# Kernel optimization log

Measured on AMD Instinct MI355X. Metric: run time of the kernel, lower is better.

The kernel has to match this reference:

```python
import jax, jax.numpy as jnp
import numpy as np

LN_EPS = 1e-5

def _layernorm(x, g, b):
    mu = jnp.mean(x, axis=-1, keepdims=True)
    var = jnp.var(x, axis=-1, keepdims=True)
    return (x - mu) * jax.lax.rsqrt(var + LN_EPS) * g + b

def setup_inputs() -> dict:
    key = jax.random.key(0)
    ks = jax.random.split(key, 5)
    N, M, A, B = 30000, 12, 256, 128
    atom_feats = jax.random.normal(ks[0], (N, A), dtype=jnp.float32)
    bond_feats = jax.random.normal(ks[1], (N, M, B), dtype=jnp.float32)
    fc_w = jax.random.normal(ks[2], (2 * A, 2 * A + B), dtype=jnp.float32) * 0.02
    fc_b = jax.random.normal(ks[3], (2 * A,), dtype=jnp.float32) * 0.02
    ln1_g = jnp.ones((2 * A,), dtype=jnp.float32)
    ln1_b = jnp.zeros((2 * A,), dtype=jnp.float32)
    ln2_g = jnp.ones((A,), dtype=jnp.float32)
    ln2_b = jnp.zeros((A,), dtype=jnp.float32)
    nbr_indices = jax.random.randint(ks[4], (N, M), 0, N, dtype=jnp.int64)
    return {"atom_feats": atom_feats, "bond_feats": bond_feats, "fc_w": fc_w,
            "fc_b": fc_b, "ln1_g": ln1_g, "ln1_b": ln1_b, "ln2_g": ln2_g,
            "ln2_b": ln2_b, "nbr_indices": nbr_indices}

def reference(atom_feats, bond_feats, fc_w, fc_b, ln1_g, ln1_b, ln2_g, ln2_b, nbr_indices):
    N, M = nbr_indices.shape
    A = atom_feats.shape[-1]
    nbr_feats = atom_feats[nbr_indices]                        # [N, M, A] gather
    atom_expand = jnp.broadcast_to(atom_feats[:, None, :], (N, M, A))
    combined = jnp.concatenate([atom_expand, nbr_feats, bond_feats], axis=-1)  # [N, M, 2A+B]
    z = jnp.einsum('nmd,kd->nmk', combined, fc_w) + fc_b       # [N, M, 2A]
    z = _layernorm(z, ln1_g, ln1_b)
    gate = jax.nn.sigmoid(z[..., :A])
    core = jax.nn.softplus(z[..., A:])
    out = jnp.mean(gate * core, axis=1)                        # [N, A]
    out = _layernorm(out, ln2_g, ln2_b)
    return atom_feats + out
```

## Files before the change

kernel.cpp:

```cpp
#include <hip/hip_runtime.h>
#include <hip/hip_bf16.h>

#define N_ATOMS 30000
#define M_NBR   12

typedef __bf16 bf16x8 __attribute__((ext_vector_type(8)));
typedef float  f32x4  __attribute__((ext_vector_type(4)));

__device__ __forceinline__ unsigned pkbf(float a, float b) {
    union { __bf16 h[2]; unsigned u; } r;
    r.h[0] = (__bf16)a; r.h[1] = (__bf16)b;
    return r.u;
}
__device__ __forceinline__ unsigned short f2bf(float f) {
    union { __bf16 h; unsigned short s; } r; r.h = (__bf16)f; return r.s;
}
__device__ __forceinline__ float bflo(unsigned u) { union { unsigned x; float f; } v; v.x = u << 16;          return v.f; }
__device__ __forceinline__ float bfhi(unsigned u) { union { unsigned x; float f; } v; v.x = u & 0xffff0000u;  return v.f; }

__device__ __forceinline__ float fexp2(float x) { return __builtin_amdgcn_exp2f(x); }
__device__ __forceinline__ float flog2(float x) { return __builtin_amdgcn_logf(x); }

__device__ __forceinline__ float rowsum16(float x) {
    union { float f; int i; } a, b;
    a.f = x;
    b.i = __builtin_amdgcn_update_dpp(0, a.i, 0x121, 0xF, 0xF, true); a.f += b.f;
    b.i = __builtin_amdgcn_update_dpp(0, a.i, 0x122, 0xF, 0xF, true); a.f += b.f;
    b.i = __builtin_amdgcn_update_dpp(0, a.i, 0x124, 0xF, 0xF, true); a.f += b.f;
    b.i = __builtin_amdgcn_update_dpp(0, a.i, 0x128, 0xF, 0xF, true); a.f += b.f;
    return a.f;
}

__device__ __forceinline__ int packAddr8(int c) {
    int cc = c & 255;
    int slot = ((cc >> 4) & 1) + ((c >> 8) << 1);
    return (cc >> 5) * 64 + (cc & 15) * 4 + slot;
}

__global__ void pack_weights(const float* __restrict__ fc_w,
                             unsigned short* __restrict__ Wp1,
                             unsigned short* __restrict__ Wp3) {
    int idx = blockIdx.x * 256 + threadIdx.x;
    const int n1 = 32 * 1024 * 8;
    if (idx < n1) {
        int j = idx & 7, n = (idx >> 3) & 1023, g = idx >> 13;
        float v = (n < 512) ? fc_w[n * 640 + g * 8 + j]
                            : fc_w[(n - 512) * 640 + 256 + g * 8 + j];
        Wp1[idx] = f2bf(v);
    } else {
        int k = idx - n1;
        if (k < 16 * 512 * 8) {
            int j = k & 7, n = (k >> 3) & 511, g = k >> 12;
            Wp3[k] = f2bf(fc_w[n * 640 + 512 + g * 8 + j]);
        }
    }
}

__global__ __launch_bounds__(512, 2) void gemm_p(
    const float* __restrict__ atom, const float* __restrict__ fc_b,
    const unsigned short* __restrict__ Wp1, unsigned short* __restrict__ P)
{
    __shared__ unsigned short sA[128 * 256];
    const int tid = threadIdx.x;
    const int r0 = blockIdx.x * 128;
    const int cb = blockIdx.y;

    #pragma unroll
    for (int s = 0; s < 8; ++s) {
        int G = tid + s * 512;
        int row = G >> 5, gc = G & 31;
        int grow = r0 + row;
        uint4 pk;
        if (grow < N_ATOMS) {
            const float4* src = reinterpret_cast<const float4*>(atom + (size_t)grow * 256 + gc * 8);
            float4 v0 = src[0], v1 = src[1];
            pk.x = pkbf(v0.x, v0.y); pk.y = pkbf(v0.z, v0.w);
            pk.z = pkbf(v1.x, v1.y); pk.w = pkbf(v1.z, v1.w);
        } else {
            pk = make_uint4(0u, 0u, 0u, 0u);
        }
        *reinterpret_cast<uint4*>(&sA[row * 256 + ((gc ^ (row & 7)) << 3)]) = pk;
    }
    __syncthreads();

    const int lane = tid & 63, wave = tid >> 6;
    const int wr = wave >> 2, wcc = wave & 3;
    const int l15 = lane & 15, l16 = lane >> 4;

    f32x4 acc[4][8];
    #pragma unroll
    for (int mt = 0; mt < 4; ++mt)
        #pragma unroll
        for (int nt = 0; nt < 8; ++nt) acc[mt][nt] = f32x4{0.f, 0.f, 0.f, 0.f};

    #pragma unroll
    for (int ks = 0; ks < 8; ++ks) {
        bf16x8 af[4];
        #pragma unroll
        for (int mt = 0; mt < 4; ++mt) {
            int row = wr * 64 + mt * 16 + l15;
            int g = ks * 4 + l16;
            af[mt] = *reinterpret_cast<const bf16x8*>(&sA[row * 256 + ((g ^ (row & 7)) << 3)]);
        }
        bf16x8 bfr[8];
        #pragma unroll
        for (int nt = 0; nt < 8; ++nt) {
            int col = cb * 512 + wcc * 128 + nt * 16 + l15;
            bfr[nt] = *reinterpret_cast<const bf16x8*>(&Wp1[((size_t)(ks * 4 + l16) * 1024 + col) * 8]);
        }
        #pragma unroll
        for (int mt = 0; mt < 4; ++mt)
            #pragma unroll
            for (int nt = 0; nt < 8; ++nt)
                acc[mt][nt] = __builtin_amdgcn_mfma_f32_16x16x32_bf16(af[mt], bfr[nt], acc[mt][nt], 0, 0, 0);
    }

    #pragma unroll
    for (int np = 0; np < 4; ++np) {
        int zc0 = wcc * 128 + np * 32 + l15;
        float b0 = (cb == 0) ? fc_b[zc0] : 0.f;
        float b1 = (cb == 0) ? fc_b[zc0 + 16] : 0.f;
        int pa = cb * 512 + packAddr8(zc0);
        #pragma unroll
        for (int mt = 0; mt < 4; ++mt) {
            #pragma unroll
            for (int j = 0; j < 4; ++j) {
                int row = r0 + wr * 64 + mt * 16 + l16 * 4 + j;
                if (row < N_ATOMS)
                    *reinterpret_cast<unsigned*>(&P[(size_t)row * 1024 + pa]) =
                        pkbf(acc[mt][2 * np][j] + b0, acc[mt][2 * np + 1][j] + b1);
            }
        }
    }
}

__global__ __launch_bounds__(256, 4) void fused_conv(
    const float* __restrict__ atom, const float* __restrict__ bond,
    const int* __restrict__ nbr, const unsigned short* __restrict__ P,
    const unsigned short* __restrict__ Wp3,
    const float* __restrict__ ln1_g, const float* __restrict__ ln1_b,
    const float* __restrict__ ln2_g, const float* __restrict__ ln2_b,
    float* __restrict__ out)
{
    __shared__ unsigned short sA[32 * 128];
    __shared__ __align__(16) float sRed[2][32][4];
    __shared__ __align__(16) float sL2[2][2][4];

    const int tid = threadIdx.x;
    const int i0 = blockIdx.x * 2;
    const int lane = tid & 63, wc = tid >> 6;
    const int l15 = lane & 15, l16 = lane >> 4;
    const float L2E = 1.4426950408889634f;
    const char* Pb = reinterpret_cast<const char*>(P);
    const unsigned cOffA = (unsigned)(wc * 256 + l15 * 8);
    const unsigned cOffB = cOffA + 128u;

    float4 bv[3];
    #pragma unroll
    for (int s = 0; s < 3; ++s) {
        int g = tid + s * 256;
        int row = g >> 5, gc = g & 31;
        bv[s] = *reinterpret_cast<const float4*>(bond + (size_t)(i0 * 12 + row) * 128 + gc * 4);
    }

    int4 nbq0 = *reinterpret_cast<const int4*>(&nbr[i0 * 12 + l16 * 4]);
    int off16 = (l16 < 2) ? (16 + l16 * 4) : 20;
    int4 nbq1 = *reinterpret_cast<const int4*>(&nbr[i0 * 12 + off16]);

    uint2 p2q[2][4][2];
    {
        const int* n0 = reinterpret_cast<const int*>(&nbq0);
        const int* n1 = reinterpret_cast<const int*>(&nbq1);
        #pragma unroll
        for (int j = 0; j < 4; ++j) {
            unsigned b0 = (unsigned)n0[j] * 2048u + 1024u;
            p2q[0][j][0] = *reinterpret_cast<const uint2*>(Pb + b0 + cOffA);
            p2q[0][j][1] = *reinterpret_cast<const uint2*>(Pb + b0 + cOffB);
            unsigned b1 = (unsigned)n1[j] * 2048u + 1024u;
            p2q[1][j][0] = *reinterpret_cast<const uint2*>(Pb + b1 + cOffA);
            p2q[1][j][1] = *reinterpret_cast<const uint2*>(Pb + b1 + cOffB);
        }
    }
    uint2 p1q[2][2];
    {
        unsigned a0 = (unsigned)(i0 + ((l16 < 3) ? 0 : 1)) * 2048u;
        p1q[0][0] = *reinterpret_cast<const uint2*>(Pb + a0 + cOffA);
        p1q[0][1] = *reinterpret_cast<const uint2*>(Pb + a0 + cOffB);
        unsigned a1 = (unsigned)(i0 + 1) * 2048u;
        p1q[1][0] = *reinterpret_cast<const uint2*>(Pb + a1 + cOffA);
        p1q[1][1] = *reinterpret_cast<const uint2*>(Pb + a1 + cOffB);
    }

    #pragma unroll
    for (int s = 0; s < 3; ++s) {
        int g = tid + s * 256;
        int row = g >> 5, gc = g & 31;
        uint2 pk;
        pk.x = pkbf(bv[s].x, bv[s].y); pk.y = pkbf(bv[s].z, bv[s].w);
        int elem = (((gc >> 1) ^ (row & 7)) << 3) + ((gc & 1) << 2);
        *reinterpret_cast<uint2*>(&sA[row * 128 + elem]) = pk;
    }
    {
        int row = 24 + (tid >> 5), gc = tid & 31;
        *reinterpret_cast<uint2*>(&sA[row * 128 + gc * 4]) = make_uint2(0u, 0u);
    }

    f32x4 acc[2][8];
    #pragma unroll
    for (int mt = 0; mt < 2; ++mt)
        #pragma unroll
        for (int np = 0; np < 2; ++np) {
            uint2 c1 = p1q[mt][np];
            float pg0 = bflo(c1.x), pg1 = bfhi(c1.x);
            float pc0 = bflo(c1.y), pc1 = bfhi(c1.y);
            #pragma unroll
            for (int j = 0; j < 4; ++j) {
                uint2 c2 = p2q[mt][j][np];
                acc[mt][np * 2 + 0][j]     = pg0 + bflo(c2.x);
                acc[mt][np * 2 + 1][j]     = pg1 + bfhi(c2.x);
                acc[mt][4 + np * 2 + 0][j] = pc0 + bflo(c2.y);
                acc[mt][4 + np * 2 + 1][j] = pc1 + bfhi(c2.y);
            }
        }
    __syncthreads();

    #pragma unroll
    for (int ks = 0; ks < 4; ++ks) {
        bf16x8 af[2];
        #pragma unroll
        for (int mt = 0; mt < 2; ++mt) {
            int row = mt * 16 + l15;
            af[mt] = *reinterpret_cast<const bf16x8*>(
                &sA[row * 128 + (((ks * 4 + l16) ^ (row & 7)) << 3)]);
        }
        #pragma unroll
        for (int p = 0; p < 2; ++p)
            #pragma unroll
            for (int np = 0; np < 2; ++np) {
                int colbase = p * 256 + wc * 64 + np * 32 + l15;
                bf16x8 b0 = *reinterpret_cast<const bf16x8*>(
                    &Wp3[((size_t)(ks * 4 + l16) * 512 + colbase) * 8]);
                bf16x8 b1 = *reinterpret_cast<const bf16x8*>(
                    &Wp3[((size_t)(ks * 4 + l16) * 512 + colbase + 16) * 8]);
                #pragma unroll
                for (int mt = 0; mt < 2; ++mt) {
                    acc[mt][p * 4 + np * 2 + 0] = __builtin_amdgcn_mfma_f32_16x16x32_bf16(
                        af[mt], b0, acc[mt][p * 4 + np * 2 + 0], 0, 0, 0);
                    acc[mt][p * 4 + np * 2 + 1] = __builtin_amdgcn_mfma_f32_16x16x32_bf16(
                        af[mt], b1, acc[mt][p * 4 + np * 2 + 1], 0, 0, 0);
                }
            }
    }

    #pragma unroll
    for (int mt = 0; mt < 2; ++mt)
        #pragma unroll
        for (int j = 0; j < 4; ++j) {
            int row = mt * 16 + l16 * 4 + j;
            float s = 0.f, q = 0.f;
            #pragma unroll
            for (int nt = 0; nt < 8; ++nt) {
                float z = acc[mt][nt][j];
                s += z; q = fmaf(z, z, q);
            }
            s = rowsum16(s);
            q = rowsum16(q);
            if (l15 == 0) { sRed[0][row][wc] = s; sRed[1][row][wc] = q; }
        }

    float g1[4], gC[4], l2b1[4], l2bC[4];
    #pragma unroll
    for (int np = 0; np < 2; ++np)
        #pragma unroll
        for (int b = 0; b < 2; ++b) {
            int nt = np * 2 + b;
            int a = wc * 64 + np * 32 + b * 16 + l15;
            g1[nt] = ln1_g[a];       l2b1[nt] = ln1_b[a] * L2E;
            gC[nt] = ln1_g[256 + a]; l2bC[nt] = ln1_b[256 + a] * L2E;
        }
    __syncthreads();

    float pa0[4] = {0.f, 0.f, 0.f, 0.f};
    float pa1[4] = {0.f, 0.f, 0.f, 0.f};
    #pragma unroll
    for (int mt = 0; mt < 2; ++mt) {
        float rs[4], mr[4];
        #pragma unroll
        for (int j = 0; j < 4; ++j) {
            int row = mt * 16 + l16 * 4 + j;
            float4 s4 = *reinterpret_cast<const float4*>(&sRed[0][row][0]);
            float4 q4 = *reinterpret_cast<const float4*>(&sRed[1][row][0]);
            float ssum = (s4.x + s4.y) + (s4.z + s4.w);
            float qsum = (q4.x + q4.y) + (q4.z + q4.w);
            float mu = ssum * (1.f / 512.f);
            float var = qsum * (1.f / 512.f) - mu * mu;
            float r = __builtin_amdgcn_rsqf(var + 1e-5f) * L2E;
            rs[j] = r; mr[j] = mu * r;
        }
        #pragma unroll
        for (int nt = 0; nt < 4; ++nt) {
            float tq = 0.f;
            #pragma unroll
            for (int j = 0; j < 4; ++j) {
                float ug = fmaf(fmaf(acc[mt][nt][j],     rs[j], -mr[j]), g1[nt], l2b1[nt]);
                float uc = fmaf(fmaf(acc[mt][nt + 4][j], rs[j], -mr[j]), gC[nt], l2bC[nt]);
                float gt  = __builtin_amdgcn_rcpf(1.f + fexp2(-ug));
                float sp2 = flog2(1.f + fexp2(uc));
                tq = fmaf(gt, sp2, tq);
            }
            if (mt == 0) {
                if (l16 < 3) pa0[nt] += tq; else pa1[nt] += tq;
            } else {
                if (l16 < 2) pa1[nt] += tq;
            }
        }
    }
    #pragma unroll
    for (int nt = 0; nt < 4; ++nt) {
        pa0[nt] += __shfl_xor(pa0[nt], 16, 64);
        pa0[nt] += __shfl_xor(pa0[nt], 32, 64);
        pa1[nt] += __shfl_xor(pa1[nt], 16, 64);
        pa1[nt] += __shfl_xor(pa1[nt], 32, 64);
    }

    {
        float s0 = (pa0[0] + pa0[1]) + (pa0[2] + pa0[3]);
        float q0 = fmaf(pa0[0], pa0[0], fmaf(pa0[1], pa0[1], fmaf(pa0[2], pa0[2], pa0[3] * pa0[3])));
        float s1 = (pa1[0] + pa1[1]) + (pa1[2] + pa1[3]);
        float q1 = fmaf(pa1[0], pa1[0], fmaf(pa1[1], pa1[1], fmaf(pa1[2], pa1[2], pa1[3] * pa1[3])));
        s0 = rowsum16(s0); q0 = rowsum16(q0);
        s1 = rowsum16(s1); q1 = rowsum16(q1);
        if (lane == 0) {
            sL2[0][0][wc] = s0; sL2[0][1][wc] = q0;
            sL2[1][0][wc] = s1; sL2[1][1][wc] = q1;
        }
    }
    __syncthreads();

    if (l16 < 2) {
        const int a = l16;
        const int gi = i0 + a;
        float4 sv = *reinterpret_cast<const float4*>(&sL2[a][0][0]);
        float4 qv = *reinterpret_cast<const float4*>(&sL2[a][1][0]);
        float ssum = (sv.x + sv.y) + (sv.z + sv.w);
        float qsum = (qv.x + qv.y) + (qv.z + qv.w);
        float mu = ssum * (1.f / 256.f);
        float var = qsum * (1.f / 256.f) - mu * mu;
        float rstd = __builtin_amdgcn_rsqf(var + 1e-5f);
        float vv[4];
        #pragma unroll
        for (int nt = 0; nt < 4; ++nt) vv[nt] = (l16 == 0) ? pa0[nt] : pa1[nt];
        #pragma unroll
        for (int np = 0; np < 2; ++np)
            #pragma unroll
            for (int b = 0; b < 2; ++b) {
                int nt = np * 2 + b;
                int c = wc * 64 + np * 32 + b * 16 + l15;
                out[(size_t)gi * 256 + c] = atom[(size_t)gi * 256 + c]
                                          + (vv[nt] - mu) * rstd * ln2_g[c] + ln2_b[c];
            }
    }
}

extern "C" void kernel_launch(void* const* d_in, const int* in_sizes, int n_in,
                              void* d_out, int out_size, void* d_ws, size_t ws_size,
                              hipStream_t stream) {
    const float* atom  = (const float*)d_in[0];
    const float* bond  = (const float*)d_in[1];
    const float* fc_w  = (const float*)d_in[2];
    const float* fc_b  = (const float*)d_in[3];
    const float* ln1_g = (const float*)d_in[4];
    const float* ln1_b = (const float*)d_in[5];
    const float* ln2_g = (const float*)d_in[6];
    const float* ln2_b = (const float*)d_in[7];
    const int*   nbr   = (const int*)d_in[8];

    char* ws = (char*)d_ws;
    unsigned short* P   = (unsigned short*)ws;
    unsigned short* Wp1 = (unsigned short*)(ws + 61440000);
    unsigned short* Wp3 = (unsigned short*)(ws + 61440000 + 524288);
    float* outp = (float*)d_out;

    hipLaunchKernelGGL(pack_weights, dim3(1280), dim3(256), 0, stream, fc_w, Wp1, Wp3);
    hipLaunchKernelGGL(gemm_p, dim3(235, 2), dim3(512), 0, stream, atom, fc_b, Wp1, P);
    hipLaunchKernelGGL(fused_conv, dim3(15000), dim3(256), 0, stream,
                       atom, bond, nbr, P, Wp3, ln1_g, ln1_b, ln2_g, ln2_b, outp);
}
```

Baseline: 239.7 us.

## Process one atom per block in fused_conv to cut registers and raise occupancy

The fused convolution kernel now handles a single atom (12 neighbor rows padded to 16) per block instead of two atoms (24 rows padded to 32). The grid doubles to 30000 blocks and the launch-bounds occupancy hint rises from 4 to 6. Accumulator and prefetch register arrays are halved and the reductions are simplified. The aim is more concurrent waves to hide gather latency. The cost is that each 16-row MFMA tile now does only 12 useful rows, against 24 of 32 before, and the weight fragments from Wp3 are reloaded twice as often per atom.

New measurement: 281.9 us. 1.18x slower.

```diff
diff --git a/kernel.cpp b/kernel.cpp
--- a/kernel.cpp
+++ b/kernel.cpp
@@ -134,7 +134,7 @@
     }
 }
 
-__global__ __launch_bounds__(256, 4) void fused_conv(
+__global__ __launch_bounds__(256, 6) void fused_conv(
     const float* __restrict__ atom, const float* __restrict__ bond,
     const int* __restrict__ nbr, const unsigned short* __restrict__ P,
     const unsigned short* __restrict__ Wp3,
@@ -142,12 +142,12 @@
     const float* __restrict__ ln2_g, const float* __restrict__ ln2_b,
     float* __restrict__ out)
 {
-    __shared__ unsigned short sA[32 * 128];
-    __shared__ __align__(16) float sRed[2][32][4];
-    __shared__ __align__(16) float sL2[2][2][4];
+    __shared__ unsigned short sA[16 * 128];
+    __shared__ __align__(16) float sRed[2][16][4];
+    __shared__ __align__(16) float sL2[2][4];
 
     const int tid = threadIdx.x;
-    const int i0 = blockIdx.x * 2;
+    const int gi = blockIdx.x;
     const int lane = tid & 63, wc = tid >> 6;
     const int l15 = lane & 15, l16 = lane >> 4;
     const float L2E = 1.4426950408889634f;
@@ -155,84 +155,71 @@
     const unsigned cOffA = (unsigned)(wc * 256 + l15 * 8);
     const unsigned cOffB = cOffA + 128u;
 
-    float4 bv[3];
-    #pragma unroll
-    for (int s = 0; s < 3; ++s) {
-        int g = tid + s * 256;
-        int row = g >> 5, gc = g & 31;
-        bv[s] = *reinterpret_cast<const float4*>(bond + (size_t)(i0 * 12 + row) * 128 + gc * 4);
-    }
-
-    int4 nbq0 = *reinterpret_cast<const int4*>(&nbr[i0 * 12 + l16 * 4]);
-    int off16 = (l16 < 2) ? (16 + l16 * 4) : 20;
-    int4 nbq1 = *reinterpret_cast<const int4*>(&nbr[i0 * 12 + off16]);
-
-    uint2 p2q[2][4][2];
-    {
-        const int* n0 = reinterpret_cast<const int*>(&nbq0);
-        const int* n1 = reinterpret_cast<const int*>(&nbq1);
+    float4 bv0, bv1;
+    {
+        int row = tid >> 5, gc = tid & 31;
+        bv0 = *reinterpret_cast<const float4*>(bond + (size_t)(gi * 12 + row) * 128 + gc * 4);
+    }
+    if (tid < 128) {
+        int g2 = tid + 256;
+        int r2 = g2 >> 5, c2 = g2 & 31;
+        bv1 = *reinterpret_cast<const float4*>(bond + (size_t)(gi * 12 + r2) * 128 + c2 * 4);
+    }
+
+    int off = (l16 < 3) ? (l16 * 4) : 8;
+    int4 nbq = *reinterpret_cast<const int4*>(&nbr[gi * 12 + off]);
+    uint2 p2q[4][2];
+    {
+        const int* nn = reinterpret_cast<const int*>(&nbq);
         #pragma unroll
         for (int j = 0; j < 4; ++j) {
-            unsigned b0 = (unsigned)n0[j] * 2048u + 1024u;
-            p2q[0][j][0] = *reinterpret_cast<const uint2*>(Pb + b0 + cOffA);
-            p2q[0][j][1] = *reinterpret_cast<const uint2*>(Pb + b0 + cOffB);
-            unsigned b1 = (unsigned)n1[j] * 2048u + 1024u;
-            p2q[1][j][0] = *reinterpret_cast<const uint2*>(Pb + b1 + cOffA);
-            p2q[1][j][1] = *reinterpret_cast<const uint2*>(Pb + b1 + cOffB);
-        }
-    }
-    uint2 p1q[2][2];
-    {
-        unsigned a0 = (unsigned)(i0 + ((l16 < 3) ? 0 : 1)) * 2048u;
-        p1q[0][0] = *reinterpret_cast<const uint2*>(Pb + a0 + cOffA);
-        p1q[0][1] = *reinterpret_cast<const uint2*>(Pb + a0 + cOffB);
-        unsigned a1 = (unsigned)(i0 + 1) * 2048u;
-        p1q[1][0] = *reinterpret_cast<const uint2*>(Pb + a1 + cOffA);
-        p1q[1][1] = *reinterpret_cast<const uint2*>(Pb + a1 + cOffB);
-    }
-
-    #pragma unroll
-    for (int s = 0; s < 3; ++s) {
-        int g = tid + s * 256;
-        int row = g >> 5, gc = g & 31;
+            unsigned b = (unsigned)nn[j] * 2048u + 1024u;
+            p2q[j][0] = *reinterpret_cast<const uint2*>(Pb + b + cOffA);
+            p2q[j][1] = *reinterpret_cast<const uint2*>(Pb + b + cOffB);
+        }
+    }
+    uint2 p1qA = *reinterpret_cast<const uint2*>(Pb + (unsigned)gi * 2048u + cOffA);
+    uint2 p1qB = *reinterpret_cast<const uint2*>(Pb + (unsigned)gi * 2048u + cOffB);
+
+    {
+        int row = tid >> 5, gc = tid & 31;
         uint2 pk;
-        pk.x = pkbf(bv[s].x, bv[s].y); pk.y = pkbf(bv[s].z, bv[s].w);
+        pk.x = pkbf(bv0.x, bv0.y); pk.y = pkbf(bv0.z, bv0.w);
         int elem = (((gc >> 1) ^ (row & 7)) << 3) + ((gc & 1) << 2);
         *reinterpret_cast<uint2*>(&sA[row * 128 + elem]) = pk;
     }
-    {
-        int row = 24 + (tid >> 5), gc = tid & 31;
-        *reinterpret_cast<uint2*>(&sA[row * 128 + gc * 4]) = make_uint2(0u, 0u);
-    }
-
-    f32x4 acc[2][8];
-    #pragma unroll
-    for (int mt = 0; mt < 2; ++mt)
-        #pragma unroll
-        for (int np = 0; np < 2; ++np) {
-            uint2 c1 = p1q[mt][np];
-            float pg0 = bflo(c1.x), pg1 = bfhi(c1.x);
-            float pc0 = bflo(c1.y), pc1 = bfhi(c1.y);
-            #pragma unroll
-            for (int j = 0; j < 4; ++j) {
-                uint2 c2 = p2q[mt][j][np];
-                acc[mt][np * 2 + 0][j]     = pg0 + bflo(c2.x);
-                acc[mt][np * 2 + 1][j]     = pg1 + bfhi(c2.x);
-                acc[mt][4 + np * 2 + 0][j] = pc0 + bflo(c2.y);
-                acc[mt][4 + np * 2 + 1][j] = pc1 + bfhi(c2.y);
-            }
-        }
+    if (tid < 128) {
+        int g2 = tid + 256;
+        int r2 = g2 >> 5, c2 = g2 & 31;
+        uint2 pk2;
+        pk2.x = pkbf(bv1.x, bv1.y); pk2.y = pkbf(bv1.z, bv1.w);
+        int e2 = (((c2 >> 1) ^ (r2 & 7)) << 3) + ((c2 & 1) << 2);
+        *reinterpret_cast<uint2*>(&sA[r2 * 128 + e2]) = pk2;
+    }
+    *reinterpret_cast<unsigned*>(&sA[1536 + tid * 2]) = 0u;
+
+    f32x4 acc[8];
+    {
+        float pg0 = bflo(p1qA.x), pg1 = bfhi(p1qA.x);
+        float pc0 = bflo(p1qA.y), pc1 = bfhi(p1qA.y);
+        float qg0 = bflo(p1qB.x), qg1 = bfhi(p1qB.x);
+        float qc0 = bflo(p1qB.y), qc1 = bfhi(p1qB.y);
+        #pragma unroll
+        for (int j = 0; j < 4; ++j) {
+            uint2 cA = p2q[j][0], cB = p2q[j][1];
+            acc[0][j] = pg0 + bflo(cA.x); acc[1][j] = pg1 + bfhi(cA.x);
+            acc[4][j] = pc0 + bflo(cA.y); acc[5][j] = pc1 + bfhi(cA.y);
+            acc[2][j] = qg0 + bflo(cB.x); acc[3][j] = qg1 + bfhi(cB.x);
+            acc[6][j] = qc0 + bflo(cB.y); acc[7][j] = qc1 + bfhi(cB.y);
+        }
+    }
     __syncthreads();
 
     #pragma unroll
     for (int ks = 0; ks < 4; ++ks) {
-        bf16x8 af[2];
-        #pragma unroll
-        for (int mt = 0; mt < 2; ++mt) {
-            int row = mt * 16 + l15;
-            af[mt] = *reinterpret_cast<const bf16x8*>(
-                &sA[row * 128 + (((ks * 4 + l16) ^ (row & 7)) << 3)]);
-        }
+        int row = l15;
+        bf16x8 af = *reinterpret_cast<const bf16x8*>(
+            &sA[row * 128 + (((ks * 4 + l16) ^ (row & 7)) << 3)]);
         #pragma unroll
         for (int p = 0; p < 2; ++p)
             #pragma unroll
@@ -242,31 +229,26 @@
                     &Wp3[((size_t)(ks * 4 + l16) * 512 + colbase) * 8]);
                 bf16x8 b1 = *reinterpret_cast<const bf16x8*>(
                     &Wp3[((size_t)(ks * 4 + l16) * 512 + colbase + 16) * 8]);
-                #pragma unroll
-                for (int mt = 0; mt < 2; ++mt) {
-                    acc[mt][p * 4 + np * 2 + 0] = __builtin_amdgcn_mfma_f32_16x16x32_bf16(
-                        af[mt], b0, acc[mt][p * 4 + np * 2 + 0], 0, 0, 0);
-                    acc[mt][p * 4 + np * 2 + 1] = __builtin_amdgcn_mfma_f32_16x16x32_bf16(
-                        af[mt], b1, acc[mt][p * 4 + np * 2 + 1], 0, 0, 0);
-                }
+                acc[p * 4 + np * 2 + 0] = __builtin_amdgcn_mfma_f32_16x16x32_bf16(
+                    af, b0, acc[p * 4 + np * 2 + 0], 0, 0, 0);
+                acc[p * 4 + np * 2 + 1] = __builtin_amdgcn_mfma_f32_16x16x32_bf16(
+                    af, b1, acc[p * 4 + np * 2 + 1], 0, 0, 0);
             }
     }
 
     #pragma unroll
-    for (int mt = 0; mt < 2; ++mt)
-        #pragma unroll
-        for (int j = 0; j < 4; ++j) {
-            int row = mt * 16 + l16 * 4 + j;
-            float s = 0.f, q = 0.f;
-            #pragma unroll
-            for (int nt = 0; nt < 8; ++nt) {
-                float z = acc[mt][nt][j];
-                s += z; q = fmaf(z, z, q);
-            }
-            s = rowsum16(s);
-            q = rowsum16(q);
-            if (l15 == 0) { sRed[0][row][wc] = s; sRed[1][row][wc] = q; }
-        }
+    for (int j = 0; j < 4; ++j) {
+        int row = l16 * 4 + j;
+        float s = 0.f, q = 0.f;
+        #pragma unroll
+        for (int nt = 0; nt < 8; ++nt) {
+            float z = acc[nt][j];
+            s += z; q = fmaf(z, z, q);
+        }
+        s = rowsum16(s);
+        q = rowsum16(q);
+        if (l15 == 0) { sRed[0][row][wc] = s; sRed[1][row][wc] = q; }
+    }
 
     float g1[4], gC[4], l2b1[4], l2bC[4];
     #pragma unroll
@@ -280,85 +262,63 @@
         }
     __syncthreads();
 
-    float pa0[4] = {0.f, 0.f, 0.f, 0.f};
-    float pa1[4] = {0.f, 0.f, 0.f, 0.f};
-    #pragma unroll
-    for (int mt = 0; mt < 2; ++mt) {
-        float rs[4], mr[4];
+    float rs[4], mr[4];
+    #pragma unroll
+    for (int j = 0; j < 4; ++j) {
+        int row = l16 * 4 + j;
+        float4 s4 = *reinterpret_cast<const float4*>(&sRed[0][row][0]);
+        float4 q4 = *reinterpret_cast<const float4*>(&sRed[1][row][0]);
+        float ssum = (s4.x + s4.y) + (s4.z + s4.w);
+        float qsum = (q4.x + q4.y) + (q4.z + q4.w);
+        float mu = ssum * (1.f / 512.f);
+        float var = qsum * (1.f / 512.f) - mu * mu;
+        float r = __builtin_amdgcn_rsqf(var + 1e-5f) * L2E;
+        rs[j] = r; mr[j] = mu * r;
+    }
+    float pa[4];
+    #pragma unroll
+    for (int nt = 0; nt < 4; ++nt) {
+        float tq = 0.f;
         #pragma unroll
         for (int j = 0; j < 4; ++j) {
-            int row = mt * 16 + l16 * 4 + j;
-            float4 s4 = *reinterpret_cast<const float4*>(&sRed[0][row][0]);
-            float4 q4 = *reinterpret_cast<const float4*>(&sRed[1][row][0]);
-            float ssum = (s4.x + s4.y) + (s4.z + s4.w);
-            float qsum = (q4.x + q4.y) + (q4.z + q4.w);
-            float mu = ssum * (1.f / 512.f);
-            float var = qsum * (1.f / 512.f) - mu * mu;
-            float r = __builtin_amdgcn_rsqf(var + 1e-5f) * L2E;
-            rs[j] = r; mr[j] = mu * r;
-        }
-        #pragma unroll
-        for (int nt = 0; nt < 4; ++nt) {
-            float tq = 0.f;
-            #pragma unroll
-            for (int j = 0; j < 4; ++j) {
-                float ug = fmaf(fmaf(acc[mt][nt][j],     rs[j], -mr[j]), g1[nt], l2b1[nt]);
-                float uc = fmaf(fmaf(acc[mt][nt + 4][j], rs[j], -mr[j]), gC[nt], l2bC[nt]);
-                float gt  = __builtin_amdgcn_rcpf(1.f + fexp2(-ug));
-                float sp2 = flog2(1.f + fexp2(uc));
-                tq = fmaf(gt, sp2, tq);
-            }
-            if (mt == 0) {
-                if (l16 < 3) pa0[nt] += tq; else pa1[nt] += tq;
-            } else {
-                if (l16 < 2) pa1[nt] += tq;
-            }
-        }
-    }
-    #pragma unroll
-    for (int nt = 0; nt < 4; ++nt) {
-        pa0[nt] += __shfl_xor(pa0[nt], 16, 64);
-        pa0[nt] += __shfl_xor(pa0[nt], 32, 64);
-        pa1[nt] += __shfl_xor(pa1[nt], 16, 64);
-        pa1[nt] += __shfl_xor(pa1[nt], 32, 64);
-    }
-
-    {
-        float s0 = (pa0[0] + pa0[1]) + (pa0[2] + pa0[3]);
-        float q0 = fmaf(pa0[0], pa0[0], fmaf(pa0[1], pa0[1], fmaf(pa0[2], pa0[2], pa0[3] * pa0[3])));
-        float s1 = (pa1[0] + pa1[1]) + (pa1[2] + pa1[3]);
-        float q1 = fmaf(pa1[0], pa1[0], fmaf(pa1[1], pa1[1], fmaf(pa1[2], pa1[2], pa1[3] * pa1[3])));
+            float ug = fmaf(fmaf(acc[nt][j],     rs[j], -mr[j]), g1[nt], l2b1[nt]);
+            float uc = fmaf(fmaf(acc[nt + 4][j], rs[j], -mr[j]), gC[nt], l2bC[nt]);
+            float gt  = __builtin_amdgcn_rcpf(1.f + fexp2(-ug));
+            float sp2 = flog2(1.f + fexp2(uc));
+            tq = fmaf(gt, sp2, tq);
+        }
+        pa[nt] = (l16 < 3) ? tq : 0.f;
+        pa[nt] += __shfl_xor(pa[nt], 16, 64);
+        pa[nt] += __shfl_xor(pa[nt], 32, 64);
+    }
+
+    {
+        float s0 = (pa[0] + pa[1]) + (pa[2] + pa[3]);
+        float q0 = fmaf(pa[0], pa[0], fmaf(pa[1], pa[1], fmaf(pa[2], pa[2], pa[3] * pa[3])));
         s0 = rowsum16(s0); q0 = rowsum16(q0);
-        s1 = rowsum16(s1); q1 = rowsum16(q1);
-        if (lane == 0) {
-            sL2[0][0][wc] = s0; sL2[0][1][wc] = q0;
-            sL2[1][0][wc] = s1; sL2[1][1][wc] = q1;
-        }
+        if (lane == 0) { sL2[0][wc] = s0; sL2[1][wc] = q0; }
     }
     __syncthreads();
 
-    if (l16 < 2) {
-        const int a = l16;
-        const int gi = i0 + a;
-        float4 sv = *reinterpret_cast<const float4*>(&sL2[a][0][0]);
-        float4 qv = *reinterpret_cast<const float4*>(&sL2[a][1][0]);
+    {
+        float4 sv = *reinterpret_cast<const float4*>(&sL2[0][0]);
+        float4 qv = *reinterpret_cast<const float4*>(&sL2[1][0]);
         float ssum = (sv.x + sv.y) + (sv.z + sv.w);
         float qsum = (qv.x + qv.y) + (qv.z + qv.w);
         float mu = ssum * (1.f / 256.f);
         float var = qsum * (1.f / 256.f) - mu * mu;
         float rstd = __builtin_amdgcn_rsqf(var + 1e-5f);
-        float vv[4];
-        #pragma unroll
-        for (int nt = 0; nt < 4; ++nt) vv[nt] = (l16 == 0) ? pa0[nt] : pa1[nt];
-        #pragma unroll
-        for (int np = 0; np < 2; ++np)
+        if (l16 == 0) {
             #pragma unroll
-            for (int b = 0; b < 2; ++b) {
-                int nt = np * 2 + b;
-                int c = wc * 64 + np * 32 + b * 16 + l15;
-                out[(size_t)gi * 256 + c] = atom[(size_t)gi * 256 + c]
-                                          + (vv[nt] - mu) * rstd * ln2_g[c] + ln2_b[c];
-            }
+            for (int np = 0; np < 2; ++np)
+                #pragma unroll
+                for (int b = 0; b < 2; ++b) {
+                    int nt = np * 2 + b;
+                    int c = wc * 64 + np * 32 + b * 16 + l15;
+                    out[(size_t)gi * 256 + c] = atom[(size_t)gi * 256 + c]
+                                              + (pa[nt] - mu) * rstd * ln2_g[c] + ln2_b[c];
+                }
+        }
     }
 }
 
@@ -383,6 +343,6 @@
 
     hipLaunchKernelGGL(pack_weights, dim3(1280), dim3(256), 0, stream, fc_w, Wp1, Wp3);
     hipLaunchKernelGGL(gemm_p, dim3(235, 2), dim3(512), 0, stream, atom, fc_b, Wp1, P);
-    hipLaunchKernelGGL(fused_conv, dim3(15000), dim3(256), 0, stream,
+    hipLaunchKernelGGL(fused_conv, dim3(30000), dim3(256), 0, stream,
                        atom, bond, nbr, P, Wp3, ln1_g, ln1_b, ln2_g, ln2_b, outp);
 }
```

## Loop fused_conv over four atom pairs, prefetching gathered rows into LDS via global_load_lds

Applied to the files above, without the earlier changes.

Each block of the fused convolution kernel now processes four consecutive atom pairs in a loop instead of one, so the grid shrinks by four. Neighbour and self rows of the precomputed projection are gathered straight into LDS with async global_load_lds, and the next pair's bond features and gathers are issued while the current pair's activation epilogue runs. This aims to hide gather latency and amortise block setup and LN parameter loads, at the cost of more LDS per block (possibly lower occupancy), fewer blocks to spread the irregular tail, and tighter reliance on barrier placement for the LDS buffer reuse.

After: 783.5 us. 227% more time.

```diff
diff --git a/kernel.cpp b/kernel.cpp
--- a/kernel.cpp
+++ b/kernel.cpp
@@ -6,6 +6,10 @@
 
 typedef __bf16 bf16x8 __attribute__((ext_vector_type(8)));
 typedef float  f32x4  __attribute__((ext_vector_type(4)));
+
+#define GLOAD_LDS16(g, l) __builtin_amdgcn_global_load_lds( \
+    (const __attribute__((address_space(1))) unsigned int*)(const void*)(g), \
+    (__attribute__((address_space(3))) unsigned int*)(void*)(l), 16, 0, 0)
 
 __device__ __forceinline__ unsigned pkbf(float a, float b) {
     union { __bf16 h[2]; unsigned u; } r;
@@ -134,6 +138,7 @@
     }
 }
 
+#define SP_STRIDE 1040
 __global__ __launch_bounds__(256, 4) void fused_conv(
     const float* __restrict__ atom, const float* __restrict__ bond,
     const int* __restrict__ nbr, const unsigned short* __restrict__ P,
@@ -143,54 +148,52 @@
     float* __restrict__ out)
 {
     __shared__ unsigned short sA[32 * 128];
+    __shared__ __align__(16) unsigned char sP[26 * SP_STRIDE];
     __shared__ __align__(16) float sRed[2][32][4];
     __shared__ __align__(16) float sL2[2][2][4];
 
     const int tid = threadIdx.x;
-    const int i0 = blockIdx.x * 2;
+    const int i00 = blockIdx.x * 8;
     const int lane = tid & 63, wc = tid >> 6;
     const int l15 = lane & 15, l16 = lane >> 4;
     const float L2E = 1.4426950408889634f;
     const char* Pb = reinterpret_cast<const char*>(P);
     const unsigned cOffA = (unsigned)(wc * 256 + l15 * 8);
     const unsigned cOffB = cOffA + 128u;
-
+    const unsigned lane16 = (unsigned)lane * 16u;
+
+    float g1[4], gC[4], l2b1[4], l2bC[4];
+    #pragma unroll
+    for (int np = 0; np < 2; ++np)
+        #pragma unroll
+        for (int b = 0; b < 2; ++b) {
+            int nt = np * 2 + b;
+            int a = wc * 64 + np * 32 + b * 16 + l15;
+            g1[nt] = ln1_g[a];       l2b1[nt] = ln1_b[a] * L2E;
+            gC[nt] = ln1_g[256 + a]; l2bC[nt] = ln1_b[256 + a] * L2E;
+        }
+
+    *reinterpret_cast<unsigned*>(&sA[3072 + tid * 4]) = 0u;
+    *reinterpret_cast<unsigned*>(&sA[3072 + 1024 + (tid & 63) * 4]) = 0u;
+
+    {
+        int ib = i00 * 12;
+        #pragma unroll
+        for (int k = 0; k < 6; ++k) {
+            int r = wc + k * 4;
+            int nb = nbr[ib + r];
+            GLOAD_LDS16(Pb + (unsigned)nb * 2048u + 1024u + lane16, &sP[r * SP_STRIDE]);
+        }
+        if (wc < 2)
+            GLOAD_LDS16(Pb + (unsigned)(i00 + wc) * 2048u + lane16, &sP[(24 + wc) * SP_STRIDE]);
+    }
     float4 bv[3];
     #pragma unroll
     for (int s = 0; s < 3; ++s) {
         int g = tid + s * 256;
         int row = g >> 5, gc = g & 31;
-        bv[s] = *reinterpret_cast<const float4*>(bond + (size_t)(i0 * 12 + row) * 128 + gc * 4);
-    }
-
-    int4 nbq0 = *reinterpret_cast<const int4*>(&nbr[i0 * 12 + l16 * 4]);
-    int off16 = (l16 < 2) ? (16 + l16 * 4) : 20;
-    int4 nbq1 = *reinterpret_cast<const int4*>(&nbr[i0 * 12 + off16]);
-
-    uint2 p2q[2][4][2];
-    {
-        const int* n0 = reinterpret_cast<const int*>(&nbq0);
-        const int* n1 = reinterpret_cast<const int*>(&nbq1);
-        #pragma unroll
-        for (int j = 0; j < 4; ++j) {
-            unsigned b0 = (unsigned)n0[j] * 2048u + 1024u;
-            p2q[0][j][0] = *reinterpret_cast<const uint2*>(Pb + b0 + cOffA);
-            p2q[0][j][1] = *reinterpret_cast<const uint2*>(Pb + b0 + cOffB);
-            unsigned b1 = (unsigned)n1[j] * 2048u + 1024u;
-            p2q[1][j][0] = *reinterpret_cast<const uint2*>(Pb + b1 + cOffA);
-            p2q[1][j][1] = *reinterpret_cast<const uint2*>(Pb + b1 + cOffB);
-        }
-    }
-    uint2 p1q[2][2];
-    {
-        unsigned a0 = (unsigned)(i0 + ((l16 < 3) ? 0 : 1)) * 2048u;
-        p1q[0][0] = *reinterpret_cast<const uint2*>(Pb + a0 + cOffA);
-        p1q[0][1] = *reinterpret_cast<const uint2*>(Pb + a0 + cOffB);
-        unsigned a1 = (unsigned)(i0 + 1) * 2048u;
-        p1q[1][0] = *reinterpret_cast<const uint2*>(Pb + a1 + cOffA);
-        p1q[1][1] = *reinterpret_cast<const uint2*>(Pb + a1 + cOffB);
-    }
-
+        bv[s] = *reinterpret_cast<const float4*>(bond + (size_t)(i00 * 12 + row) * 128 + gc * 4);
+    }
     #pragma unroll
     for (int s = 0; s < 3; ++s) {
         int g = tid + s * 256;
@@ -200,165 +203,189 @@
         int elem = (((gc >> 1) ^ (row & 7)) << 3) + ((gc & 1) << 2);
         *reinterpret_cast<uint2*>(&sA[row * 128 + elem]) = pk;
     }
-    {
-        int row = 24 + (tid >> 5), gc = tid & 31;
-        *reinterpret_cast<uint2*>(&sA[row * 128 + gc * 4]) = make_uint2(0u, 0u);
-    }
-
-    f32x4 acc[2][8];
-    #pragma unroll
-    for (int mt = 0; mt < 2; ++mt)
-        #pragma unroll
-        for (int np = 0; np < 2; ++np) {
-            uint2 c1 = p1q[mt][np];
-            float pg0 = bflo(c1.x), pg1 = bfhi(c1.x);
-            float pc0 = bflo(c1.y), pc1 = bfhi(c1.y);
+    __syncthreads();
+
+    for (int t = 0; t < 4; ++t) {
+        const int i0 = i00 + t * 2;
+
+        f32x4 acc[2][8];
+        #pragma unroll
+        for (int mt = 0; mt < 2; ++mt) {
+            int zr0 = mt * 16 + l16 * 4;
+            int p1row = 24 + ((zr0 >= 12) ? 1 : 0);
+            uint2 c1A = *reinterpret_cast<const uint2*>(&sP[p1row * SP_STRIDE + cOffA]);
+            uint2 c1B = *reinterpret_cast<const uint2*>(&sP[p1row * SP_STRIDE + cOffB]);
+            float pg0 = bflo(c1A.x), pg1 = bfhi(c1A.x);
+            float pc0 = bflo(c1A.y), pc1 = bfhi(c1A.y);
+            float qg0 = bflo(c1B.x), qg1 = bfhi(c1B.x);
+            float qc0 = bflo(c1B.y), qc1 = bfhi(c1B.y);
             #pragma unroll
             for (int j = 0; j < 4; ++j) {
-                uint2 c2 = p2q[mt][j][np];
-                acc[mt][np * 2 + 0][j]     = pg0 + bflo(c2.x);
-                acc[mt][np * 2 + 1][j]     = pg1 + bfhi(c2.x);
-                acc[mt][4 + np * 2 + 0][j] = pc0 + bflo(c2.y);
-                acc[mt][4 + np * 2 + 1][j] = pc1 + bfhi(c2.y);
-            }
-        }
-    __syncthreads();
-
-    #pragma unroll
-    for (int ks = 0; ks < 4; ++ks) {
-        bf16x8 af[2];
+                int zrow = zr0 + j;
+                int r = (zrow < 24) ? zrow : 23;
+                uint2 cA = *reinterpret_cast<const uint2*>(&sP[r * SP_STRIDE + cOffA]);
+                uint2 cB = *reinterpret_cast<const uint2*>(&sP[r * SP_STRIDE + cOffB]);
+                acc[mt][0][j] = pg0 + bflo(cA.x); acc[mt][1][j] = pg1 + bfhi(cA.x);
+                acc[mt][4][j] = pc0 + bflo(cA.y); acc[mt][5][j] = pc1 + bfhi(cA.y);
+                acc[mt][2][j] = qg0 + bflo(cB.x); acc[mt][3][j] = qg1 + bfhi(cB.x);
+                acc[mt][6][j] = qc0 + bflo(cB.y); acc[mt][7][j] = qc1 + bfhi(cB.y);
+            }
+        }
+
+        #pragma unroll
+        for (int ks = 0; ks < 4; ++ks) {
+            bf16x8 af[2];
+            #pragma unroll
+            for (int mt = 0; mt < 2; ++mt) {
+                int row = mt * 16 + l15;
+                af[mt] = *reinterpret_cast<const bf16x8*>(
+                    &sA[row * 128 + (((ks * 4 + l16) ^ (row & 7)) << 3)]);
+            }
+            #pragma unroll
+            for (int p = 0; p < 2; ++p)
+                #pragma unroll
+                for (int np = 0; np < 2; ++np) {
+                    int colbase = p * 256 + wc * 64 + np * 32 + l15;
+                    bf16x8 b0 = *reinterpret_cast<const bf16x8*>(
+                        &Wp3[((size_t)(ks * 4 + l16) * 512 + colbase) * 8]);
+                    bf16x8 b1 = *reinterpret_cast<const bf16x8*>(
+                        &Wp3[((size_t)(ks * 4 + l16) * 512 + colbase + 16) * 8]);
+                    #pragma unroll
+                    for (int mt = 0; mt < 2; ++mt) {
+                        acc[mt][p * 4 + np * 2 + 0] = __builtin_amdgcn_mfma_f32_16x16x32_bf16(
+                            af[mt], b0, acc[mt][p * 4 + np * 2 + 0], 0, 0, 0);
+                        acc[mt][p * 4 + np * 2 + 1] = __builtin_amdgcn_mfma_f32_16x16x32_bf16(
+                            af[mt], b1, acc[mt][p * 4 + np * 2 + 1], 0, 0, 0);
+                    }
+                }
+        }
+
+        #pragma unroll
+        for (int mt = 0; mt < 2; ++mt)
+            #pragma unroll
+            for (int j = 0; j < 4; ++j) {
+                int row = mt * 16 + l16 * 4 + j;
+                float s = 0.f, q = 0.f;
+                #pragma unroll
+                for (int nt = 0; nt < 8; ++nt) {
+                    float z = acc[mt][nt][j];
+                    s += z; q = fmaf(z, z, q);
+                }
+                s = rowsum16(s);
+                q = rowsum16(q);
+                if (l15 == 0) { sRed[0][row][wc] = s; sRed[1][row][wc] = q; }
+            }
+        __syncthreads();
+
+        if (t < 3) {
+            const int i1 = i0 + 2;
+            #pragma unroll
+            for (int s = 0; s < 3; ++s) {
+                int g = tid + s * 256;
+                int row = g >> 5, gc = g & 31;
+                bv[s] = *reinterpret_cast<const float4*>(bond + (size_t)(i1 * 12 + row) * 128 + gc * 4);
+            }
+            int ib = i1 * 12;
+            #pragma unroll
+            for (int k = 0; k < 6; ++k) {
+                int r = wc + k * 4;
+                int nb = nbr[ib + r];
+                GLOAD_LDS16(Pb + (unsigned)nb * 2048u + 1024u + lane16, &sP[r * SP_STRIDE]);
+            }
+            if (wc < 2)
+                GLOAD_LDS16(Pb + (unsigned)(i1 + wc) * 2048u + lane16, &sP[(24 + wc) * SP_STRIDE]);
+        }
+
+        float pa0[4] = {0.f, 0.f, 0.f, 0.f};
+        float pa1[4] = {0.f, 0.f, 0.f, 0.f};
         #pragma unroll
         for (int mt = 0; mt < 2; ++mt) {
-            int row = mt * 16 + l15;
-            af[mt] = *reinterpret_cast<const bf16x8*>(
-                &sA[row * 128 + (((ks * 4 + l16) ^ (row & 7)) << 3)]);
-        }
-        #pragma unroll
-        for (int p = 0; p < 2; ++p)
-            #pragma unroll
-            for (int np = 0; np < 2; ++np) {
-                int colbase = p * 256 + wc * 64 + np * 32 + l15;
-                bf16x8 b0 = *reinterpret_cast<const bf16x8*>(
-                    &Wp3[((size_t)(ks * 4 + l16) * 512 + colbase) * 8]);
-                bf16x8 b1 = *reinterpret_cast<const bf16x8*>(
-                    &Wp3[((size_t)(ks * 4 + l16) * 512 + colbase + 16) * 8]);
+            float rs[4], mr[4];
+            #pragma unroll
+            for (int j = 0; j < 4; ++j) {
+                int row = mt * 16 + l16 * 4 + j;
+                float4 s4 = *reinterpret_cast<const float4*>(&sRed[0][row][0]);
+                float4 q4 = *reinterpret_cast<const float4*>(&sRed[1][row][0]);
+                float ssum = (s4.x + s4.y) + (s4.z + s4.w);
+                float qsum = (q4.x + q4.y) + (q4.z + q4.w);
+                float mu = ssum * (1.f / 512.f);
+                float var = qsum * (1.f / 512.f) - mu * mu;
+                float r = __builtin_amdgcn_rsqf(var + 1e-5f) * L2E;
+                rs[j] = r; mr[j] = mu * r;
+            }
+            #pragma unroll
+            for (int nt = 0; nt < 4; ++nt) {
+                float tq = 0.f;
                 #pragma unroll
-                for (int mt = 0; mt < 2; ++mt) {
-                    acc[mt][p * 4 + np * 2 + 0] = __builtin_amdgcn_mfma_f32_16x16x32_bf16(
-                        af[mt], b0, acc[mt][p * 4 + np * 2 + 0], 0, 0, 0);
-                    acc[mt][p * 4 + np * 2 + 1] = __builtin_amdgcn_mfma_f32_16x16x32_bf16(
-                        af[mt], b1, acc[mt][p * 4 + np * 2 + 1], 0, 0, 0);
+                for (int j = 0; j < 4; ++j) {
+                    float ug = fmaf(fmaf(acc[mt][nt][j],     rs[j], -mr[j]), g1[nt], l2b1[nt]);
+                    float uc = fmaf(fmaf(acc[mt][nt + 4][j], rs[j], -mr[j]), gC[nt], l2bC[nt]);
+                    float gt  = __builtin_amdgcn_rcpf(1.f + fexp2(-ug));
+                    float sp2 = flog2(1.f + fexp2(uc));
+                    tq = fmaf(gt, sp2, tq);
                 }
-            }
-    }
-
-    #pragma unroll
-    for (int mt = 0; mt < 2; ++mt)
-        #pragma unroll
-        for (int j = 0; j < 4; ++j) {
-            int row = mt * 16 + l16 * 4 + j;
-            float s = 0.f, q = 0.f;
-            #pragma unroll
-            for (int nt = 0; nt < 8; ++nt) {
-                float z = acc[mt][nt][j];
-                s += z; q = fmaf(z, z, q);
-            }
-            s = rowsum16(s);
-            q = rowsum16(q);
-            if (l15 == 0) { sRed[0][row][wc] = s; sRed[1][row][wc] = q; }
-        }
-
-    float g1[4], gC[4], l2b1[4], l2bC[4];
-    #pragma unroll
-    for (int np = 0; np < 2; ++np)
-        #pragma unroll
-        for (int b = 0; b < 2; ++b) {
-            int nt = np * 2 + b;
-            int a = wc * 64 + np * 32 + b * 16 + l15;
-            g1[nt] = ln1_g[a];       l2b1[nt] = ln1_b[a] * L2E;
-            gC[nt] = ln1_g[256 + a]; l2bC[nt] = ln1_b[256 + a] * L2E;
-        }
-    __syncthreads();
-
-    float pa0[4] = {0.f, 0.f, 0.f, 0.f};
-    float pa1[4] = {0.f, 0.f, 0.f, 0.f};
-    #pragma unroll
-    for (int mt = 0; mt < 2; ++mt) {
-        float rs[4], mr[4];
-        #pragma unroll
-        for (int j = 0; j < 4; ++j) {
-            int row = mt * 16 + l16 * 4 + j;
-            float4 s4 = *reinterpret_cast<const float4*>(&sRed[0][row][0]);
-            float4 q4 = *reinterpret_cast<const float4*>(&sRed[1][row][0]);
-            float ssum = (s4.x + s4.y) + (s4.z + s4.w);
-            float qsum = (q4.x + q4.y) + (q4.z + q4.w);
-            float mu = ssum * (1.f / 512.f);
-            float var = qsum * (1.f / 512.f) - mu * mu;
-            float r = __builtin_amdgcn_rsqf(var + 1e-5f) * L2E;
-            rs[j] = r; mr[j] = mu * r;
+                if (mt == 0) {
+                    if (l16 < 3) pa0[nt] += tq; else pa1[nt] += tq;
+                } else {
+                    if (l16 < 2) pa1[nt] += tq;
+                }
+            }
         }
         #pragma unroll
         for (int nt = 0; nt < 4; ++nt) {
-            float tq = 0.f;
-            #pragma unroll
-            for (int j = 0; j < 4; ++j) {
-                float ug = fmaf(fmaf(acc[mt][nt][j],     rs[j], -mr[j]), g1[nt], l2b1[nt]);
-                float uc = fmaf(fmaf(acc[mt][nt + 4][j], rs[j], -mr[j]), gC[nt], l2bC[nt]);
-                float gt  = __builtin_amdgcn_rcpf(1.f + fexp2(-ug));
-                float sp2 = flog2(1.f + fexp2(uc));
-                tq = fmaf(gt, sp2, tq);
-            }
-            if (mt == 0) {
-                if (l16 < 3) pa0[nt] += tq; else pa1[nt] += tq;
-            } else {
-                if (l16 < 2) pa1[nt] += tq;
-            }
-        }
-    }
-    #pragma unroll
-    for (int nt = 0; nt < 4; ++nt) {
-        pa0[nt] += __shfl_xor(pa0[nt], 16, 64);
-        pa0[nt] += __shfl_xor(pa0[nt], 32, 64);
-        pa1[nt] += __shfl_xor(pa1[nt], 16, 64);
-        pa1[nt] += __shfl_xor(pa1[nt], 32, 64);
-    }
-
-    {
-        float s0 = (pa0[0] + pa0[1]) + (pa0[2] + pa0[3]);
-        float q0 = fmaf(pa0[0], pa0[0], fmaf(pa0[1], pa0[1], fmaf(pa0[2], pa0[2], pa0[3] * pa0[3])));
-        float s1 = (pa1[0] + pa1[1]) + (pa1[2] + pa1[3]);
-        float q1 = fmaf(pa1[0], pa1[0], fmaf(pa1[1], pa1[1], fmaf(pa1[2], pa1[2], pa1[3] * pa1[3])));
-        s0 = rowsum16(s0); q0 = rowsum16(q0);
-        s1 = rowsum16(s1); q1 = rowsum16(q1);
-        if (lane == 0) {
-            sL2[0][0][wc] = s0; sL2[0][1][wc] = q0;
-            sL2[1][0][wc] = s1; sL2[1][1][wc] = q1;
-        }
-    }
-    __syncthreads();
-
-    if (l16 < 2) {
-        const int a = l16;
-        const int gi = i0 + a;
-        float4 sv = *reinterpret_cast<const float4*>(&sL2[a][0][0]);
-        float4 qv = *reinterpret_cast<const float4*>(&sL2[a][1][0]);
-        float ssum = (sv.x + sv.y) + (sv.z + sv.w);
-        float qsum = (qv.x + qv.y) + (qv.z + qv.w);
-        float mu = ssum * (1.f / 256.f);
-        float var = qsum * (1.f / 256.f) - mu * mu;
-        float rstd = __builtin_amdgcn_rsqf(var + 1e-5f);
-        float vv[4];
-        #pragma unroll
-        for (int nt = 0; nt < 4; ++nt) vv[nt] = (l16 == 0) ? pa0[nt] : pa1[nt];
-        #pragma unroll
-        for (int np = 0; np < 2; ++np)
-            #pragma unroll
-            for (int b = 0; b < 2; ++b) {
-                int nt = np * 2 + b;
-                int c = wc * 64 + np * 32 + b * 16 + l15;
-                out[(size_t)gi * 256 + c] = atom[(size_t)gi * 256 + c]
-                                          + (vv[nt] - mu) * rstd * ln2_g[c] + ln2_b[c];
-            }
+            pa0[nt] += __shfl_xor(pa0[nt], 16, 64);
+            pa0[nt] += __shfl_xor(pa0[nt], 32, 64);
+            pa1[nt] += __shfl_xor(pa1[nt], 16, 64);
+            pa1[nt] += __shfl_xor(pa1[nt], 32, 64);
+        }
+
+        if (t < 3) {
+            #pragma unroll
+            for (int s = 0; s < 3; ++s) {
+                int g = tid + s * 256;
+                int row = g >> 5, gc = g & 31;
+                uint2 pk;
+                pk.x = pkbf(bv[s].x, bv[s].y); pk.y = pkbf(bv[s].z, bv[s].w);
+                int elem = (((gc >> 1) ^ (row & 7)) << 3) + ((gc & 1) << 2);
+                *reinterpret_cast<uint2*>(&sA[row * 128 + elem]) = pk;
+            }
+        }
+
+        {
+            float s0 = (pa0[0] + pa0[1]) + (pa0[2] + pa0[3]);
+            float q0 = fmaf(pa0[0], pa0[0], fmaf(pa0[1], pa0[1], fmaf(pa0[2], pa0[2], pa0[3] * pa0[3])));
+            float s1 = (pa1[0] + pa1[1]) + (pa1[2] + pa1[3]);
+            float q1 = fmaf(pa1[0], pa1[0], fmaf(pa1[1], pa1[1], fmaf(pa1[2], pa1[2], pa1[3] * pa1[3])));
+            s0 = rowsum16(s0); q0 = rowsum16(q0);
+            s1 = rowsum16(s1); q1 = rowsum16(q1);
+            if (lane == 0) {
+                sL2[0][0][wc] = s0; sL2[0][1][wc] = q0;
+                sL2[1][0][wc] = s1; sL2[1][1][wc] = q1;
+            }
+        }
+        __syncthreads();
+
+        if (l16 < 2) {
+            const int a = l16;
+            const int gi = i0 + a;
+            float4 sv = *reinterpret_cast<const float4*>(&sL2[a][0][0]);
+            float4 qv = *reinterpret_cast<const float4*>(&sL2[a][1][0]);
+            float ssum = (sv.x + sv.y) + (sv.z + sv.w);
+            float qsum = (qv.x + qv.y) + (qv.z + qv.w);
+            float mu = ssum * (1.f / 256.f);
+            float var = qsum * (1.f / 256.f) - mu * mu;
+            float rstd = __builtin_amdgcn_rsqf(var + 1e-5f);
+            #pragma unroll
+            for (int np = 0; np < 2; ++np)
+                #pragma unroll
+                for (int b = 0; b < 2; ++b) {
+                    int nt = np * 2 + b;
+                    int c = wc * 64 + np * 32 + b * 16 + l15;
+                    float vv = (a == 0) ? pa0[nt] : pa1[nt];
+                    out[(size_t)gi * 256 + c] = atom[(size_t)gi * 256 + c]
+                                              + (vv - mu) * rstd * ln2_g[c] + ln2_b[c];
+                }
+        }
     }
 }
 
@@ -383,6 +410,6 @@
 
     hipLaunchKernelGGL(pack_weights, dim3(1280), dim3(256), 0, stream, fc_w, Wp1, Wp3);
     hipLaunchKernelGGL(gemm_p, dim3(235, 2), dim3(512), 0, stream, atom, fc_b, Wp1, P);
-    hipLaunchKernelGGL(fused_conv, dim3(15000), dim3(256), 0, stream,
+    hipLaunchKernelGGL(fused_conv, dim3(3750), dim3(256), 0, stream,
                        atom, bond, nbr, P, Wp3, ln1_g, ln1_b, ln2_g, ln2_b, outp);
 }
```
